# Kernel optimization log

Measured on AMD Instinct MI355X. Metric: run time of the kernel, lower is better.

## Reference

```python
import jax, jax.numpy as jnp
import numpy as np

B, N, D_IN, D_OUT = 4, 2048, 1024, 1024

def setup_inputs() -> dict:
    key = jax.random.key(0)
    ks = jax.random.split(key, 7)
    s_in = 1.0 / np.sqrt(D_IN)
    return {
        "X": jax.random.normal(ks[0], (B, N, D_IN), dtype=jnp.float32),
        "Wq": jax.random.uniform(ks[1], (D_IN, D_OUT), jnp.float32, -s_in, s_in),
        "bq": jax.random.uniform(ks[2], (D_OUT,), jnp.float32, -s_in, s_in),
        "Wk": jax.random.uniform(ks[3], (D_IN, D_OUT), jnp.float32, -s_in, s_in),
        "bk": jax.random.uniform(ks[4], (D_OUT,), jnp.float32, -s_in, s_in),
        "Wv": jax.random.uniform(ks[5], (D_IN, D_OUT), jnp.float32, -s_in, s_in),
        "bv": jax.random.uniform(ks[6], (D_OUT,), jnp.float32, -s_in, s_in),
    }

def reference(X, Wq, bq, Wk, bk, Wv, bv):
    # QKV projections: [B,N,D_in] @ [D_in,D_out] -> [B,N,D_out]
    q = jnp.einsum('bnd,de->bne', X, Wq) + bq
    k = jnp.einsum('bnd,de->bne', X, Wk) + bk
    v = jnp.einsum('bnd,de->bne', X, Wv) + bv
    # Unscaled attention (faithful: original has no 1/sqrt(d))
    scores = jnp.einsum('bne,bme->bnm', q, k)  # [B,N,N]
    weights = jax.nn.softmax(scores, axis=-1)
    return jnp.einsum('bnm,bme->bne', weights, v)
```

## Files before the change

### kernel.cpp

```cpp
#include <hip/hip_runtime.h>
#include <hip/hip_bf16.h>
#include <hip/hip_fp16.h>
#include <stdint.h>
#include <math.h>


typedef unsigned short ushort_t;
typedef __attribute__((ext_vector_type(8))) _Float16  f16x8;
typedef __attribute__((ext_vector_type(4))) _Float16  f16x4;
typedef __attribute__((ext_vector_type(4))) float     f32x4;

__device__ __forceinline__ void async_load16(const void* g, void* l) {
  __builtin_amdgcn_global_load_lds(
      (const __attribute__((address_space(1))) void*)g,
      (__attribute__((address_space(3))) void*)l, 16, 0, 0);
}

__global__ __launch_bounds__(256)
void qkv_gemm_kernel(const ushort_t* __restrict__ A, const ushort_t* __restrict__ BT,
                     const float* __restrict__ bq, const float* __restrict__ bk,
                     const float* __restrict__ bvp,
                     __half* __restrict__ Qh, __half* __restrict__ Kh,
                     ushort_t* __restrict__ Vt)
{
  const int K = 1024;
  __shared__ ushort_t As[2][128 * 32];
  __shared__ ushort_t Bs[2][128 * 32];

  const int t    = threadIdx.x;
  const int lane = t & 63;
  const int wave = t >> 6;
  const int wm   = (wave >> 1) * 64;
  const int wn   = (wave & 1) * 64;

  const ushort_t* Ab = A + (long)blockIdx.y * 128 * K;
  const ushort_t* Bb = BT + (long)blockIdx.x * 128 * K;

  const int ldr = t >> 2;
  const int swzs = (ldr & 3) ^ ((ldr >> 2) & 3);
  const int ldc = ((t & 3) ^ swzs) * 8;
  const int frow = lane & 15;
  const int fsz  = (frow & 3) ^ ((frow >> 2) & 3);
  const int fo   = (((lane >> 4) ^ fsz)) * 8;

  f32x4 acc[4][4];
  const f32x4 zero = {0.0f, 0.0f, 0.0f, 0.0f};
#pragma unroll
  for (int i = 0; i < 4; ++i)
#pragma unroll
    for (int j = 0; j < 4; ++j) acc[i][j] = zero;

  for (int k0 = 0; k0 < K; k0 += 64) {
    __syncthreads();
    const ushort_t* ga = Ab + (long)ldr * K + k0 + ldc;
    const ushort_t* gb = Bb + (long)ldr * K + k0 + ldc;
#pragma unroll
    for (int h = 0; h < 2; ++h) {
      async_load16(ga + h * 32,                &As[h][t * 8]);
      async_load16(ga + h * 32 + 64 * (long)K, &As[h][2048 + t * 8]);
      async_load16(gb + h * 32,                &Bs[h][t * 8]);
      async_load16(gb + h * 32 + 64 * (long)K, &Bs[h][2048 + t * 8]);
    }
    __syncthreads();
#pragma unroll
    for (int h = 0; h < 2; ++h) {
      f16x8 af[4], bf[4];
#pragma unroll
      for (int i = 0; i < 4; ++i) {
        af[i] = *(const f16x8*)&As[h][(wm + i * 16 + frow) * 32 + fo];
        bf[i] = *(const f16x8*)&Bs[h][(wn + i * 16 + frow) * 32 + fo];
      }
#pragma unroll
      for (int mi = 0; mi < 4; ++mi)
#pragma unroll
        for (int ni = 0; ni < 4; ++ni)
          acc[mi][ni] = __builtin_amdgcn_mfma_f32_16x16x32_f16(af[mi], bf[ni], acc[mi][ni], 0, 0, 0);
    }
  }

  const int er = (lane >> 4) * 4;
  const int ec = lane & 15;
  const int tgt = blockIdx.x >> 3;
  const float* bias = (tgt == 0) ? bq : (tgt == 1) ? bk : bvp;
#pragma unroll
  for (int ni = 0; ni < 4; ++ni) {
    const int c = (blockIdx.x & 7) * 128 + wn + ni * 16 + ec;
    const float bval = bias[c];
#pragma unroll
    for (int mi = 0; mi < 4; ++mi) {
      const long grow0 = (long)blockIdx.y * 128 + wm + mi * 16 + er;
      if (tgt < 2) {
        __half* o = (tgt == 0) ? Qh : Kh;
#pragma unroll
        for (int r = 0; r < 4; ++r)
          o[(grow0 + r) * 1024 + c] = __float2half(acc[mi][ni][r] + bval);
      } else {
        const long b  = grow0 >> 11;
        const long ml = grow0 & 2047;
        f16x4 v4;
#pragma unroll
        for (int r = 0; r < 4; ++r) v4[r] = (_Float16)(acc[mi][ni][r] + bval);
        *(f16x4*)&Vt[b * 2097152 + (long)c * 2048 + ml] = v4;
      }
    }
  }
}

__global__ __launch_bounds__(256)
void qk_gemm_kernel(const ushort_t* __restrict__ Q, const ushort_t* __restrict__ Kh,
                    __half* __restrict__ S, float* __restrict__ PM, float* __restrict__ PS)
{
  const int K = 1024;
  __shared__ ushort_t As[2][128 * 32];
  __shared__ ushort_t Bs[2][128 * 32];

  const int t    = threadIdx.x;
  const int lane = t & 63;
  const int wave = t >> 6;
  const int wm   = (wave >> 1) * 64;
  const int wn   = (wave & 1) * 64;
  const long z   = blockIdx.z;

  const ushort_t* Ab = Q + z * 2048 * 1024 + (long)blockIdx.y * 128 * K;
  const ushort_t* Bb = Kh + z * 2048 * 1024 + (long)blockIdx.x * 128 * K;
  __half* Sb = S + z * 2048 * 2048;

  const int ldr = t >> 2;
  const int swzs = (ldr & 3) ^ ((ldr >> 2) & 3);
  const int ldc = ((t & 3) ^ swzs) * 8;
  const int frow = lane & 15;
  const int fsz  = (frow & 3) ^ ((frow >> 2) & 3);
  const int fo   = (((lane >> 4) ^ fsz)) * 8;

  f32x4 acc[4][4];
  const f32x4 zero = {0.0f, 0.0f, 0.0f, 0.0f};
#pragma unroll
  for (int i = 0; i < 4; ++i)
#pragma unroll
    for (int j = 0; j < 4; ++j) acc[i][j] = zero;

  for (int k0 = 0; k0 < K; k0 += 64) {
    __syncthreads();
    const ushort_t* ga = Ab + (long)ldr * K + k0 + ldc;
    const ushort_t* gb = Bb + (long)ldr * K + k0 + ldc;
#pragma unroll
    for (int h = 0; h < 2; ++h) {
      async_load16(ga + h * 32,                &As[h][t * 8]);
      async_load16(ga + h * 32 + 64 * (long)K, &As[h][2048 + t * 8]);
      async_load16(gb + h * 32,                &Bs[h][t * 8]);
      async_load16(gb + h * 32 + 64 * (long)K, &Bs[h][2048 + t * 8]);
    }
    __syncthreads();
#pragma unroll
    for (int h = 0; h < 2; ++h) {
      f16x8 af[4], bf[4];
#pragma unroll
      for (int i = 0; i < 4; ++i) {
        af[i] = *(const f16x8*)&As[h][(wm + i * 16 + frow) * 32 + fo];
        bf[i] = *(const f16x8*)&Bs[h][(wn + i * 16 + frow) * 32 + fo];
      }
#pragma unroll
      for (int mi = 0; mi < 4; ++mi)
#pragma unroll
        for (int ni = 0; ni < 4; ++ni)
          acc[mi][ni] = __builtin_amdgcn_mfma_f32_16x16x32_f16(af[mi], bf[ni], acc[mi][ni], 0, 0, 0);
    }
  }

  const int er = (lane >> 4) * 4;
  const int ec = lane & 15;
  const int cc = blockIdx.x * 2 + (wave & 1);
  float* PMb = PM + z * 32 * 2048 + (long)cc * 2048;
  float* PSb = PS + z * 32 * 2048 + (long)cc * 2048;

#pragma unroll
  for (int mi = 0; mi < 4; ++mi)
#pragma unroll
    for (int r = 0; r < 4; ++r) {
      float m = fmaxf(fmaxf(acc[mi][0][r], acc[mi][1][r]),
                      fmaxf(acc[mi][2][r], acc[mi][3][r]));
      m = fmaxf(m, __shfl_xor(m, 1));
      m = fmaxf(m, __shfl_xor(m, 2));
      m = fmaxf(m, __shfl_xor(m, 4));
      m = fmaxf(m, __shfl_xor(m, 8));
      float s = 0.0f;
#pragma unroll
      for (int ni = 0; ni < 4; ++ni) {
        const float e = __expf(acc[mi][ni][r] - m);
        acc[mi][ni][r] = e;
        s += e;
      }
      s += __shfl_xor(s, 1);
      s += __shfl_xor(s, 2);
      s += __shfl_xor(s, 4);
      s += __shfl_xor(s, 8);
      if (ec == 0) {
        const long row = (long)blockIdx.y * 128 + wm + mi * 16 + er + r;
        PMb[row] = m;
        PSb[row] = s;
      }
    }

#pragma unroll
  for (int ni = 0; ni < 4; ++ni) {
    const long col = (long)blockIdx.x * 128 + wn + ni * 16 + ec;
#pragma unroll
    for (int mi = 0; mi < 4; ++mi)
#pragma unroll
      for (int r = 0; r < 4; ++r) {
        const long grow = (long)blockIdx.y * 128 + wm + mi * 16 + er + r;
        Sb[grow * 2048 + col] = __float2half(acc[mi][ni][r]);
      }
  }
}

__global__ __launch_bounds__(256)
void softmax_reduce_kernel(const float* __restrict__ PM, const float* __restrict__ PS,
                           float* __restrict__ Sc)
{
  const int r = blockIdx.x * 256 + threadIdx.x;
  const int b = r >> 11, row = r & 2047;
  const long base = (long)b * 32 * 2048 + row;
  float m = -3.4e38f;
#pragma unroll
  for (int cb = 0; cb < 32; ++cb) m = fmaxf(m, PM[base + cb * 2048]);
  float l = 0.0f;
#pragma unroll
  for (int cb = 0; cb < 32; ++cb) l += PS[base + cb * 2048] * __expf(PM[base + cb * 2048] - m);
  const float inv = 1.0f / l;
#pragma unroll
  for (int cb = 0; cb < 32; ++cb) Sc[base + cb * 2048] = __expf(PM[base + cb * 2048] - m) * inv;
}

__global__ __launch_bounds__(256)
void pv_gemm_kernel(const ushort_t* __restrict__ S, const ushort_t* __restrict__ Vt,
                    const float* __restrict__ Sc, float* __restrict__ Out)
{
  const int K = 2048;
  __shared__ ushort_t As[2][128 * 32];
  __shared__ ushort_t Bs[2][128 * 32];

  const int t    = threadIdx.x;
  const int lane = t & 63;
  const int wave = t >> 6;
  const int wm   = (wave >> 1) * 64;
  const int wn   = (wave & 1) * 64;
  const long z   = blockIdx.z;

  const ushort_t* Ab = S + z * 2048 * 2048 + (long)blockIdx.y * 128 * K;
  const ushort_t* Bb = Vt + z * 1024 * 2048 + (long)blockIdx.x * 128 * K;
  const float* Scb = Sc + z * 32 * 2048;
  float* Cb = Out + z * 2048 * 1024;

  const int ldr = t >> 2;
  const int swzs = (ldr & 3) ^ ((ldr >> 2) & 3);
  const int ldc = ((t & 3) ^ swzs) * 8;
  const int frow = lane & 15;
  const int fsz  = (frow & 3) ^ ((frow >> 2) & 3);
  const int fo   = (((lane >> 4) ^ fsz)) * 8;

  const int arow0 = blockIdx.y * 128 + wm + frow;

  f32x4 acc[4][4];
  const f32x4 zero = {0.0f, 0.0f, 0.0f, 0.0f};
#pragma unroll
  for (int i = 0; i < 4; ++i)
#pragma unroll
    for (int j = 0; j < 4; ++j) acc[i][j] = zero;

  for (int k0 = 0; k0 < K; k0 += 64) {
    const int cb = k0 >> 6;
    _Float16 sc16[4];
#pragma unroll
    for (int i = 0; i < 4; ++i)
      sc16[i] = (_Float16)Scb[(long)cb * 2048 + arow0 + i * 16];

    __syncthreads();
    const ushort_t* ga = Ab + (long)ldr * K + k0 + ldc;
    const ushort_t* gb = Bb + (long)ldr * K + k0 + ldc;
#pragma unroll
    for (int h = 0; h < 2; ++h) {
      async_load16(ga + h * 32,                &As[h][t * 8]);
      async_load16(ga + h * 32 + 64 * (long)K, &As[h][2048 + t * 8]);
      async_load16(gb + h * 32,                &Bs[h][t * 8]);
      async_load16(gb + h * 32 + 64 * (long)K, &Bs[h][2048 + t * 8]);
    }
    __syncthreads();
#pragma unroll
    for (int h = 0; h < 2; ++h) {
      f16x8 af[4], bf[4];
#pragma unroll
      for (int i = 0; i < 4; ++i) {
        af[i] = *(const f16x8*)&As[h][(wm + i * 16 + frow) * 32 + fo] * sc16[i];
        bf[i] = *(const f16x8*)&Bs[h][(wn + i * 16 + frow) * 32 + fo];
      }
#pragma unroll
      for (int mi = 0; mi < 4; ++mi)
#pragma unroll
        for (int ni = 0; ni < 4; ++ni)
          acc[mi][ni] = __builtin_amdgcn_mfma_f32_16x16x32_f16(af[mi], bf[ni], acc[mi][ni], 0, 0, 0);
    }
  }

  const int er = (lane >> 4) * 4;
  const int ec = lane & 15;
#pragma unroll
  for (int ni = 0; ni < 4; ++ni) {
    const int gcol = blockIdx.x * 128 + wn + ni * 16 + ec;
#pragma unroll
    for (int mi = 0; mi < 4; ++mi) {
#pragma unroll
      for (int r = 0; r < 4; ++r) {
        const long grow = (long)blockIdx.y * 128 + wm + mi * 16 + er + r;
        Cb[grow * 1024 + gcol] = acc[mi][ni][r];
      }
    }
  }
}

__global__ __launch_bounds__(256)
void cvt_f32_f16_kernel(const float* __restrict__ src, __half* __restrict__ dst, long n)
{
  const long i = ((long)blockIdx.x * 256 + threadIdx.x) * 8;
  if (i + 8 > n) return;
  const float4 a = *(const float4*)(src + i);
  const float4 b = *(const float4*)(src + i + 4);
  f16x8 h;
  h[0] = (_Float16)a.x; h[1] = (_Float16)a.y; h[2] = (_Float16)a.z; h[3] = (_Float16)a.w;
  h[4] = (_Float16)b.x; h[5] = (_Float16)b.y; h[6] = (_Float16)b.z; h[7] = (_Float16)b.w;
  *(f16x8*)((ushort_t*)dst + i) = h;
}

__global__ __launch_bounds__(256)
void transpose_cvt3_kernel(const float* __restrict__ W0, const float* __restrict__ W1,
                           const float* __restrict__ W2, __half* __restrict__ dst)
{
  __shared__ float tile[32][33];
  const int z = blockIdx.z;
  const float* src = (z == 0) ? W0 : (z == 1) ? W1 : W2;
  __half* d = dst + (long)z * 1024 * 1024;
  const int c0 = blockIdx.x * 32;
  const int r0 = blockIdx.y * 32;
  const int tx = threadIdx.x & 31;
  const int ty = threadIdx.x >> 5;
#pragma unroll
  for (int i = 0; i < 32; i += 8)
    tile[ty + i][tx] = src[(long)(r0 + ty + i) * 1024 + (c0 + tx)];
  __syncthreads();
#pragma unroll
  for (int i = 0; i < 32; i += 8)
    d[(long)(c0 + ty + i) * 1024 + (r0 + tx)] = __float2half(tile[tx][ty + i]);
}

extern "C" void kernel_launch(void* const* d_in, const int* in_sizes, int n_in,
                              void* d_out, int out_size, void* d_ws, size_t ws_size,
                              hipStream_t stream)
{
  const int  Bb = 4, Nn = 2048, Dd = 1024;
  const long BN = (long)Bb * Nn;

  const float* X  = (const float*)d_in[0];
  const float* Wq = (const float*)d_in[1];
  const float* bq = (const float*)d_in[2];
  const float* Wk = (const float*)d_in[3];
  const float* bk = (const float*)d_in[4];
  const float* Wv = (const float*)d_in[5];
  const float* bv = (const float*)d_in[6];
  float* Out      = (float*)d_out;

  uint8_t* w = (uint8_t*)d_ws;
  ushort_t* Wt = (ushort_t*)w;  w += (size_t)3 * Dd * Dd * 2;

  transpose_cvt3_kernel<<<dim3(Dd / 32, Dd / 32, 3), 256, 0, stream>>>(Wq, Wk, Wv, (__half*)Wt);

  const size_t statsBytes = (size_t)Bb * 32 * Nn * 4;
  const size_t fullNeed = (size_t)3 * Dd * Dd * 2
                        + 4 * ((size_t)BN * Dd * 2)
                        + (size_t)Bb * Nn * Nn * 2
                        + 3 * statsBytes;

  if (ws_size >= fullNeed) {
    ushort_t* Xh = (ushort_t*)w;  w += (size_t)BN * Dd * 2;
    ushort_t* Q  = (ushort_t*)w;  w += (size_t)BN * Dd * 2;
    ushort_t* Kb = (ushort_t*)w;  w += (size_t)BN * Dd * 2;
    ushort_t* Vt = (ushort_t*)w;  w += (size_t)BN * Dd * 2;
    ushort_t* S  = (ushort_t*)w;  w += (size_t)Bb * Nn * Nn * 2;
    float*    PM = (float*)w;     w += statsBytes;
    float*    PS = (float*)w;     w += statsBytes;
    float*    Sc = (float*)w;

    cvt_f32_f16_kernel<<<dim3((unsigned)(BN * Dd / (8 * 256))), 256, 0, stream>>>(
        X, (__half*)Xh, BN * Dd);

    qkv_gemm_kernel<<<dim3(3 * Dd / 128, BN / 128, 1), 256, 0, stream>>>(
        Xh, Wt, bq, bk, bv, (__half*)Q, (__half*)Kb, Vt);

    qk_gemm_kernel<<<dim3(Nn / 128, Nn / 128, Bb), 256, 0, stream>>>(
        Q, Kb, (__half*)S, PM, PS);

    softmax_reduce_kernel<<<dim3((unsigned)(Bb * Nn / 256)), 256, 0, stream>>>(PM, PS, Sc);

    pv_gemm_kernel<<<dim3(Dd / 128, Nn / 128, Bb), 256, 0, stream>>>(
        S, Vt, Sc, Out);
  } else {
    ushort_t* Xh = (ushort_t*)w;  w += (size_t)Nn * Dd * 2;
    ushort_t* Q  = (ushort_t*)w;  w += (size_t)Nn * Dd * 2;
    ushort_t* Kb = (ushort_t*)w;  w += (size_t)Nn * Dd * 2;
    ushort_t* Vt = (ushort_t*)w;  w += (size_t)Nn * Dd * 2;
    ushort_t* S  = (ushort_t*)w;  w += (size_t)Nn * Nn * 2;
    float*    PM = (float*)w;     w += (size_t)32 * Nn * 4;
    float*    PS = (float*)w;     w += (size_t)32 * Nn * 4;
    float*    Sc = (float*)w;

    for (int b = 0; b < Bb; ++b) {
      const float* Xb = X + (long)b * Nn * Dd;
      cvt_f32_f16_kernel<<<dim3((unsigned)((long)Nn * Dd / (8 * 256))), 256, 0, stream>>>(
          Xb, (__half*)Xh, (long)Nn * Dd);
      qkv_gemm_kernel<<<dim3(3 * Dd / 128, Nn / 128, 1), 256, 0, stream>>>(
          Xh, Wt, bq, bk, bv, (__half*)Q, (__half*)Kb, Vt);
      qk_gemm_kernel<<<dim3(Nn / 128, Nn / 128, 1), 256, 0, stream>>>(
          Q, Kb, (__half*)S, PM, PS);
      softmax_reduce_kernel<<<dim3((unsigned)(Nn / 256)), 256, 0, stream>>>(PM, PS, Sc);
      pv_gemm_kernel<<<dim3(Dd / 128, Nn / 128, 1), 256, 0, stream>>>(
          S, Vt, Sc, Out + (long)b * Nn * Dd);
    }
  }
}
```

Before: 273.6 us.

## Fold Q and K projections into a single Wq·Wkᵀ product and drop row-constant bias terms

The scores are rewritten as X·(Wq Wkᵀ)·Xᵀ plus a per-key-column term X·(Wk bq). The query-side bias terms are constant along each softmax row and are dropped. The projection GEMM now computes Z = X·M and V only, 2/3 of the old output width, after a small 1024³ GEMM forms M. A GEMV builds the column bias, which is added before the softmax statistics. Forming M in fp16 and then multiplying by X changes rounding, and the unscaled scores may be large, which risks accuracy loss. The extra small kernels add launch overhead.

```diff
diff --git a/kernel.cpp b/kernel.cpp
--- a/kernel.cpp
+++ b/kernel.cpp
@@ -17,11 +17,9 @@
 }
 
 __global__ __launch_bounds__(256)
-void qkv_gemm_kernel(const ushort_t* __restrict__ A, const ushort_t* __restrict__ BT,
-                     const float* __restrict__ bq, const float* __restrict__ bk,
-                     const float* __restrict__ bvp,
-                     __half* __restrict__ Qh, __half* __restrict__ Kh,
-                     ushort_t* __restrict__ Vt)
+void zv_gemm_kernel(const ushort_t* __restrict__ A, const ushort_t* __restrict__ BT,
+                    const float* __restrict__ bvp,
+                    __half* __restrict__ Zh, ushort_t* __restrict__ Vt)
 {
   const int K = 1024;
   __shared__ ushort_t As[2][128 * 32];
@@ -81,20 +79,18 @@
   const int er = (lane >> 4) * 4;
   const int ec = lane & 15;
   const int tgt = blockIdx.x >> 3;
-  const float* bias = (tgt == 0) ? bq : (tgt == 1) ? bk : bvp;
 #pragma unroll
   for (int ni = 0; ni < 4; ++ni) {
     const int c = (blockIdx.x & 7) * 128 + wn + ni * 16 + ec;
-    const float bval = bias[c];
 #pragma unroll
     for (int mi = 0; mi < 4; ++mi) {
       const long grow0 = (long)blockIdx.y * 128 + wm + mi * 16 + er;
-      if (tgt < 2) {
-        __half* o = (tgt == 0) ? Qh : Kh;
+      if (tgt == 0) {
 #pragma unroll
         for (int r = 0; r < 4; ++r)
-          o[(grow0 + r) * 1024 + c] = __float2half(acc[mi][ni][r] + bval);
+          Zh[(grow0 + r) * 1024 + c] = __float2half(acc[mi][ni][r]);
       } else {
+        const float bval = bvp[c];
         const long b  = grow0 >> 11;
         const long ml = grow0 & 2047;
         f16x4 v4;
@@ -107,7 +103,82 @@
 }
 
 __global__ __launch_bounds__(256)
-void qk_gemm_kernel(const ushort_t* __restrict__ Q, const ushort_t* __restrict__ Kh,
+void gemm_f16_kernel(const ushort_t* __restrict__ A, const ushort_t* __restrict__ BT,
+                     __half* __restrict__ C)
+{
+  const int K = 1024;
+  __shared__ ushort_t As[2][128 * 32];
+  __shared__ ushort_t Bs[2][128 * 32];
+
+  const int t    = threadIdx.x;
+  const int lane = t & 63;
+  const int wave = t >> 6;
+  const int wm   = (wave >> 1) * 64;
+  const int wn   = (wave & 1) * 64;
+
+  const ushort_t* Ab = A + (long)blockIdx.y * 128 * K;
+  const ushort_t* Bb = BT + (long)blockIdx.x * 128 * K;
+
+  const int ldr = t >> 2;
+  const int swzs = (ldr & 3) ^ ((ldr >> 2) & 3);
+  const int ldc = ((t & 3) ^ swzs) * 8;
+  const int frow = lane & 15;
+  const int fsz  = (frow & 3) ^ ((frow >> 2) & 3);
+  const int fo   = (((lane >> 4) ^ fsz)) * 8;
+
+  f32x4 acc[4][4];
+  const f32x4 zero = {0.0f, 0.0f, 0.0f, 0.0f};
+#pragma unroll
+  for (int i = 0; i < 4; ++i)
+#pragma unroll
+    for (int j = 0; j < 4; ++j) acc[i][j] = zero;
+
+  for (int k0 = 0; k0 < K; k0 += 64) {
+    __syncthreads();
+    const ushort_t* ga = Ab + (long)ldr * K + k0 + ldc;
+    const ushort_t* gb = Bb + (long)ldr * K + k0 + ldc;
+#pragma unroll
+    for (int h = 0; h < 2; ++h) {
+      async_load16(ga + h * 32,                &As[h][t * 8]);
+      async_load16(ga + h * 32 + 64 * (long)K, &As[h][2048 + t * 8]);
+      async_load16(gb + h * 32,                &Bs[h][t * 8]);
+      async_load16(gb + h * 32 + 64 * (long)K, &Bs[h][2048 + t * 8]);
+    }
+    __syncthreads();
+#pragma unroll
+    for (int h = 0; h < 2; ++h) {
+      f16x8 af[4], bf[4];
+#pragma unroll
+      for (int i = 0; i < 4; ++i) {
+        af[i] = *(const f16x8*)&As[h][(wm + i * 16 + frow) * 32 + fo];
+        bf[i] = *(const f16x8*)&Bs[h][(wn + i * 16 + frow) * 32 + fo];
+      }
+#pragma unroll
+      for (int mi = 0; mi < 4; ++mi)
+#pragma unroll
+        for (int ni = 0; ni < 4; ++ni)
+          acc[mi][ni] = __builtin_amdgcn_mfma_f32_16x16x32_f16(af[mi], bf[ni], acc[mi][ni], 0, 0, 0);
+    }
+  }
+
+  const int er = (lane >> 4) * 4;
+  const int ec = lane & 15;
+#pragma unroll
+  for (int ni = 0; ni < 4; ++ni) {
+    const int gcol = blockIdx.x * 128 + wn + ni * 16 + ec;
+#pragma unroll
+    for (int mi = 0; mi < 4; ++mi)
+#pragma unroll
+      for (int r = 0; r < 4; ++r) {
+        const long grow = (long)blockIdx.y * 128 + wm + mi * 16 + er + r;
+        C[grow * 1024 + gcol] = __float2half(acc[mi][ni][r]);
+      }
+  }
+}
+
+__global__ __launch_bounds__(256)
+void qk_gemm_kernel(const ushort_t* __restrict__ Z, const ushort_t* __restrict__ Xh,
+                    const float* __restrict__ Cc,
                     __half* __restrict__ S, float* __restrict__ PM, float* __restrict__ PS)
 {
   const int K = 1024;
@@ -121,8 +192,8 @@
   const int wn   = (wave & 1) * 64;
   const long z   = blockIdx.z;
 
-  const ushort_t* Ab = Q + z * 2048 * 1024 + (long)blockIdx.y * 128 * K;
-  const ushort_t* Bb = Kh + z * 2048 * 1024 + (long)blockIdx.x * 128 * K;
+  const ushort_t* Ab = Z + z * 2048 * 1024 + (long)blockIdx.y * 128 * K;
+  const ushort_t* Bb = Xh + z * 2048 * 1024 + (long)blockIdx.x * 128 * K;
   __half* Sb = S + z * 2048 * 2048;
 
   const int ldr = t >> 2;
@@ -169,6 +240,17 @@
 
   const int er = (lane >> 4) * 4;
   const int ec = lane & 15;
+
+  const float* Ccb = Cc + z * 2048;
+#pragma unroll
+  for (int ni = 0; ni < 4; ++ni) {
+    const float cbv = Ccb[blockIdx.x * 128 + wn + ni * 16 + ec];
+#pragma unroll
+    for (int mi = 0; mi < 4; ++mi)
+#pragma unroll
+      for (int r = 0; r < 4; ++r) acc[mi][ni][r] += cbv;
+  }
+
   const int cc = blockIdx.x * 2 + (wave & 1);
   float* PMb = PM + z * 32 * 2048 + (long)cc * 2048;
   float* PSb = PS + z * 32 * 2048 + (long)cc * 2048;
@@ -319,6 +401,43 @@
 }
 
 __global__ __launch_bounds__(256)
+void prep_kernel(const float* __restrict__ X, __half* __restrict__ Xh, int nx,
+                 const float* __restrict__ Wq, __half* __restrict__ Wqh,
+                 const float* __restrict__ Wk, __half* __restrict__ Wkh,
+                 const float* __restrict__ Wv, __half* __restrict__ Wvt)
+{
+  const int bid = blockIdx.x;
+  const int tid = threadIdx.x;
+  if (bid < nx + 1024) {
+    const float* src; __half* dst; long base;
+    if (bid < nx)          { src = X;  dst = Xh;  base = (long)bid * 2048; }
+    else if (bid < nx+512) { src = Wq; dst = Wqh; base = (long)(bid - nx) * 2048; }
+    else                   { src = Wk; dst = Wkh; base = (long)(bid - nx - 512) * 2048; }
+    const long i = base + (long)tid * 8;
+    const float4 a = *(const float4*)(src + i);
+    const float4 b = *(const float4*)(src + i + 4);
+    f16x8 h;
+    h[0] = (_Float16)a.x; h[1] = (_Float16)a.y; h[2] = (_Float16)a.z; h[3] = (_Float16)a.w;
+    h[4] = (_Float16)b.x; h[5] = (_Float16)b.y; h[6] = (_Float16)b.z; h[7] = (_Float16)b.w;
+    *(f16x8*)((ushort_t*)dst + i) = h;
+  } else {
+    __shared__ float tile[32][33];
+    const int t2 = bid - (nx + 1024);
+    const int c0 = (t2 & 31) * 32;
+    const int r0 = (t2 >> 5) * 32;
+    const int tx = tid & 31;
+    const int ty = tid >> 5;
+#pragma unroll
+    for (int i = 0; i < 32; i += 8)
+      tile[ty + i][tx] = Wv[(long)(r0 + ty + i) * 1024 + (c0 + tx)];
+    __syncthreads();
+#pragma unroll
+    for (int i = 0; i < 32; i += 8)
+      Wvt[(long)(c0 + ty + i) * 1024 + (r0 + tx)] = __float2half(tile[tx][ty + i]);
+  }
+}
+
+__global__ __launch_bounds__(256)
 void cvt_f32_f16_kernel(const float* __restrict__ src, __half* __restrict__ dst, long n)
 {
   const long i = ((long)blockIdx.x * 256 + threadIdx.x) * 8;
@@ -332,24 +451,38 @@
 }
 
 __global__ __launch_bounds__(256)
-void transpose_cvt3_kernel(const float* __restrict__ W0, const float* __restrict__ W1,
-                           const float* __restrict__ W2, __half* __restrict__ dst)
-{
-  __shared__ float tile[32][33];
-  const int z = blockIdx.z;
-  const float* src = (z == 0) ? W0 : (z == 1) ? W1 : W2;
-  __half* d = dst + (long)z * 1024 * 1024;
-  const int c0 = blockIdx.x * 32;
-  const int r0 = blockIdx.y * 32;
-  const int tx = threadIdx.x & 31;
-  const int ty = threadIdx.x >> 5;
-#pragma unroll
-  for (int i = 0; i < 32; i += 8)
-    tile[ty + i][tx] = src[(long)(r0 + ty + i) * 1024 + (c0 + tx)];
-  __syncthreads();
-#pragma unroll
-  for (int i = 0; i < 32; i += 8)
-    d[(long)(c0 + ty + i) * 1024 + (r0 + tx)] = __float2half(tile[tx][ty + i]);
+void wkbq_kernel(const float* __restrict__ Wk, const float* __restrict__ bq,
+                 float* __restrict__ wkbq)
+{
+  const int d = blockIdx.x * 256 + threadIdx.x;
+  const float* row = Wk + (long)d * 1024;
+  float acc = 0.0f;
+  for (int e = 0; e < 1024; e += 4) {
+    const float4 wv = *(const float4*)(row + e);
+    const float4 bv = *(const float4*)(bq + e);
+    acc += wv.x * bv.x + wv.y * bv.y + wv.z * bv.z + wv.w * bv.w;
+  }
+  wkbq[d] = acc;
+}
+
+__global__ __launch_bounds__(256)
+void cgemv_kernel(const ushort_t* __restrict__ Xh, const float* __restrict__ wkbq,
+                  float* __restrict__ c)
+{
+  const int wave = threadIdx.x >> 6, lane = threadIdx.x & 63;
+  const long row = (long)blockIdx.x * 4 + wave;
+  const ushort_t* xr = Xh + row * 1024 + lane * 16;
+  const f16x8 a0 = *(const f16x8*)xr;
+  const f16x8 a1 = *(const f16x8*)(xr + 8);
+  const float* wb = wkbq + lane * 16;
+  float acc = 0.0f;
+#pragma unroll
+  for (int j = 0; j < 8; ++j) acc += (float)a0[j] * wb[j];
+#pragma unroll
+  for (int j = 0; j < 8; ++j) acc += (float)a1[j] * wb[j + 8];
+#pragma unroll
+  for (int off = 32; off > 0; off >>= 1) acc += __shfl_xor(acc, off, 64);
+  if (lane == 0) c[row] = acc;
 }
 
 extern "C" void kernel_launch(void* const* d_in, const int* in_sizes, int n_in,
@@ -363,64 +496,77 @@
   const float* Wq = (const float*)d_in[1];
   const float* bq = (const float*)d_in[2];
   const float* Wk = (const float*)d_in[3];
-  const float* bk = (const float*)d_in[4];
+  const float* bk = (const float*)d_in[4];  (void)bk;
   const float* Wv = (const float*)d_in[5];
   const float* bv = (const float*)d_in[6];
   float* Out      = (float*)d_out;
 
   uint8_t* w = (uint8_t*)d_ws;
-  ushort_t* Wt = (ushort_t*)w;  w += (size_t)3 * Dd * Dd * 2;
-
-  transpose_cvt3_kernel<<<dim3(Dd / 32, Dd / 32, 3), 256, 0, stream>>>(Wq, Wk, Wv, (__half*)Wt);
+  ushort_t* Wqh   = (ushort_t*)w;  w += (size_t)Dd * Dd * 2;
+  ushort_t* Wkh   = (ushort_t*)w;  w += (size_t)Dd * Dd * 2;
+  ushort_t* MtWvt = (ushort_t*)w;  w += (size_t)2 * Dd * Dd * 2;
+  ushort_t* Mt  = MtWvt;
+  ushort_t* Wvt = MtWvt + (size_t)Dd * Dd;
+  float* wkbq = (float*)w;  w += (size_t)Dd * 4;
+  float* cvec = (float*)w;  w += (size_t)BN * 4;
 
   const size_t statsBytes = (size_t)Bb * 32 * Nn * 4;
-  const size_t fullNeed = (size_t)3 * Dd * Dd * 2
-                        + 4 * ((size_t)BN * Dd * 2)
+  const size_t fullNeed = (size_t)8 * Dd * Dd * 2 + Dd * 4 + BN * 4
+                        + 3 * ((size_t)BN * Dd * 2)
                         + (size_t)Bb * Nn * Nn * 2
                         + 3 * statsBytes;
 
+  wkbq_kernel<<<dim3(Dd / 256), 256, 0, stream>>>(Wk, bq, wkbq);
+
   if (ws_size >= fullNeed) {
     ushort_t* Xh = (ushort_t*)w;  w += (size_t)BN * Dd * 2;
-    ushort_t* Q  = (ushort_t*)w;  w += (size_t)BN * Dd * 2;
-    ushort_t* Kb = (ushort_t*)w;  w += (size_t)BN * Dd * 2;
+    ushort_t* Zh = (ushort_t*)w;  w += (size_t)BN * Dd * 2;
     ushort_t* Vt = (ushort_t*)w;  w += (size_t)BN * Dd * 2;
     ushort_t* S  = (ushort_t*)w;  w += (size_t)Bb * Nn * Nn * 2;
     float*    PM = (float*)w;     w += statsBytes;
     float*    PS = (float*)w;     w += statsBytes;
     float*    Sc = (float*)w;
 
-    cvt_f32_f16_kernel<<<dim3((unsigned)(BN * Dd / (8 * 256))), 256, 0, stream>>>(
-        X, (__half*)Xh, BN * Dd);
-
-    qkv_gemm_kernel<<<dim3(3 * Dd / 128, BN / 128, 1), 256, 0, stream>>>(
-        Xh, Wt, bq, bk, bv, (__half*)Q, (__half*)Kb, Vt);
+    const int nx = (int)(BN * Dd / 2048);
+    prep_kernel<<<dim3(nx + 2048), 256, 0, stream>>>(
+        X, (__half*)Xh, nx, Wq, (__half*)Wqh, Wk, (__half*)Wkh, Wv, (__half*)Wvt);
+
+    gemm_f16_kernel<<<dim3(Dd / 128, Dd / 128), 256, 0, stream>>>(Wkh, Wqh, (__half*)Mt);
+
+    cgemv_kernel<<<dim3((unsigned)(BN / 4)), 256, 0, stream>>>(Xh, wkbq, cvec);
+
+    zv_gemm_kernel<<<dim3(2 * Dd / 128, BN / 128), 256, 0, stream>>>(
+        Xh, MtWvt, bv, (__half*)Zh, Vt);
 
     qk_gemm_kernel<<<dim3(Nn / 128, Nn / 128, Bb), 256, 0, stream>>>(
-        Q, Kb, (__half*)S, PM, PS);
+        Zh, Xh, cvec, (__half*)S, PM, PS);
 
     softmax_reduce_kernel<<<dim3((unsigned)(Bb * Nn / 256)), 256, 0, stream>>>(PM, PS, Sc);
 
-    pv_gemm_kernel<<<dim3(Dd / 128, Nn / 128, Bb), 256, 0, stream>>>(
-        S, Vt, Sc, Out);
+    pv_gemm_kernel<<<dim3(Dd / 128, Nn / 128, Bb), 256, 0, stream>>>(S, Vt, Sc, Out);
   } else {
     ushort_t* Xh = (ushort_t*)w;  w += (size_t)Nn * Dd * 2;
-    ushort_t* Q  = (ushort_t*)w;  w += (size_t)Nn * Dd * 2;
-    ushort_t* Kb = (ushort_t*)w;  w += (size_t)Nn * Dd * 2;
+    ushort_t* Zh = (ushort_t*)w;  w += (size_t)Nn * Dd * 2;
     ushort_t* Vt = (ushort_t*)w;  w += (size_t)Nn * Dd * 2;
     ushort_t* S  = (ushort_t*)w;  w += (size_t)Nn * Nn * 2;
     float*    PM = (float*)w;     w += (size_t)32 * Nn * 4;
     float*    PS = (float*)w;     w += (size_t)32 * Nn * 4;
     float*    Sc = (float*)w;
 
+    prep_kernel<<<dim3(2048), 256, 0, stream>>>(
+        nullptr, nullptr, 0, Wq, (__half*)Wqh, Wk, (__half*)Wkh, Wv, (__half*)Wvt);
+    gemm_f16_kernel<<<dim3(Dd / 128, Dd / 128), 256, 0, stream>>>(Wkh, Wqh, (__half*)Mt);
+
     for (int b = 0; b < Bb; ++b) {
       const float* Xb = X + (long)b * Nn * Dd;
       cvt_f32_f16_kernel<<<dim3((unsigned)((long)Nn * Dd / (8 * 256))), 256, 0, stream>>>(
           Xb, (__half*)Xh, (long)Nn * Dd);
-      qkv_gemm_kernel<<<dim3(3 * Dd / 128, Nn / 128, 1), 256, 0, stream>>>(
-          Xh, Wt, bq, bk, bv, (__half*)Q, (__half*)Kb, Vt);
+      cgemv_kernel<<<dim3(Nn / 4), 256, 0, stream>>>(Xh, wkbq, cvec);
+      zv_gemm_kernel<<<dim3(2 * Dd / 128, Nn / 128), 256, 0, stream>>>(
+          Xh, MtWvt, bv, (__half*)Zh, Vt);
       qk_gemm_kernel<<<dim3(Nn / 128, Nn / 128, 1), 256, 0, stream>>>(
-          Q, Kb, (__half*)S, PM, PS);
-      softmax_reduce_kernel<<<dim3((unsigned)(Nn / 256)), 256, 0, stream>>>(PM, PS, Sc);
+          Zh, Xh, cvec, (__half*)S, PM, PS);
+      softmax_reduce_kernel<<<dim3(Nn / 256), 256, 0, stream>>>(PM, PS, Sc);
       pv_gemm_kernel<<<dim3(Dd / 128, Nn / 128, 1), 256, 0, stream>>>(
           S, Vt, Sc, Out + (long)b * Nn * Dd);
     }
```

Measured after the change: 326.1 us. 19.2% more time.
